# Kernel optimization log

Hardware: AMD Instinct MI355X
Metric: run time of the kernel (lower is better)

Reference implementation:

```python
import jax, jax.numpy as jnp
import numpy as np

B, LQ, D, H, NL, NP, DFF = 8, 1800, 256, 8, 4, 4, 1024
DH = D // H
SHAPES = np.array([[100, 150], [50, 75], [25, 38], [13, 19]], dtype=np.int64)
LIN = int((SHAPES[:, 0] * SHAPES[:, 1]).sum())
QN, QP = -8.0, 7.0  # 4-bit signed LSQ


def lsq(w, alpha):
    """LSQ weight quantization (per-tensor scale, STE round/grad-scale)."""
    g = 1.0 / jnp.sqrt(w.size * QP)
    a = alpha * g + jax.lax.stop_gradient(alpha - alpha * g)  # grad-scaled alpha
    wn = jnp.clip(w / a, QN, QP)
    wq = wn + jax.lax.stop_gradient(jnp.round(wn) - wn)       # round with STE
    return wq * a


def linear_q(x, w, b, a):
    return x @ lsq(w, a).T + b


def layer_norm(x, g, b, eps=1e-5):
    m = x.mean(-1, keepdims=True)
    v = ((x - m) ** 2).mean(-1, keepdims=True)
    return (x - m) / jnp.sqrt(v + eps) * g + b


def setup_inputs():
    key = jax.random.key(0)
    ks = list(jax.random.split(key, 20))

    def nrm(i, shape, s=0.02):
        return jax.random.normal(ks[i], shape, jnp.float32) * s

    def alpha(w):
        return 2.0 * jnp.mean(jnp.abs(w)) / jnp.sqrt(QP)

    qW, kW, vW, oW = nrm(0, (D, D)), nrm(1, (D, D)), nrm(2, (D, D)), nrm(3, (D, D))
    val_W = nrm(4, (D, D))
    off_W = nrm(5, (H * NL * NP * 2, D))
    aw_W = nrm(6, (H * NL * NP, D))
    out_W = nrm(7, (D, D))
    W1, W2 = nrm(8, (DFF, D)), nrm(9, (D, DFF))
    lsi = np.concatenate([[0], np.cumsum(SHAPES[:, 0] * SHAPES[:, 1])[:-1]]).astype(np.int64)
    z = jnp.zeros
    return dict(
        tgt=nrm(10, (B, LQ, D), 1.0),
        query_pos=nrm(11, (B, LQ, D), 1.0),
        reference_points=jax.random.uniform(ks[12], (B, LQ, NL, 2), jnp.float32),
        src=nrm(13, (B, LIN, D), 1.0),
        qW=qW, qb=z(D), kW=kW, kb=z(D), vW=vW, vb=z(D), oW=oW, ob=z(D),
        a_q=alpha(qW), a_k=alpha(kW), a_v=alpha(vW), a_o=alpha(oW),
        val_W=val_W, val_b=z(D), a_val=alpha(val_W),
        off_W=off_W, off_b=z(H * NL * NP * 2),
        aw_W=aw_W, aw_b=z(H * NL * NP),
        out_W=out_W, out_b=z(D), a_out=alpha(out_W),
        W1=W1, b1=z(DFF), a_w1=alpha(W1),
        W2=W2, b2=z(D), a_w2=alpha(W2),
        ln1_g=jnp.ones(D), ln1_b=z(D),
        ln2_g=jnp.ones(D), ln2_b=z(D),
        ln3_g=jnp.ones(D), ln3_b=z(D),
        src_spatial_shapes=jnp.asarray(SHAPES),
        level_start_index=jnp.asarray(lsi),
        src_padding_mask=jnp.zeros((B, LIN), dtype=bool),
    )


def reference(tgt, query_pos, reference_points, src,
              qW, qb, kW, kb, vW, vb, oW, ob, a_q, a_k, a_v, a_o,
              val_W, val_b, a_val, off_W, off_b, aw_W, aw_b, out_W, out_b, a_out,
              W1, b1, a_w1, W2, b2, a_w2,
              ln1_g, ln1_b, ln2_g, ln2_b, ln3_g, ln3_b,
              src_spatial_shapes, level_start_index, src_padding_mask):
    shapes = np.asarray(src_spatial_shapes)  # static spatial shapes per level

    # ---- quantized self-attention (dropout = eval mode, i.e. identity) ----
    qk_in = tgt + query_pos
    q = linear_q(qk_in, qW, qb, a_q).reshape(B, LQ, H, DH)
    k = linear_q(qk_in, kW, kb, a_k).reshape(B, LQ, H, DH)
    v = linear_q(tgt, vW, vb, a_v).reshape(B, LQ, H, DH)
    scores = jnp.einsum('bqhd,bkhd->bhqk', q, k) / jnp.sqrt(jnp.float32(DH))
    p = jax.nn.softmax(scores, axis=-1)
    sa = jnp.einsum('bhqk,bkhd->bqhd', p, v).reshape(B, LQ, D)
    tgt = layer_norm(tgt + linear_q(sa, oW, ob, a_o), ln2_g, ln2_b)

    # ---- quantized multi-scale deformable cross-attention ----
    query = tgt + query_pos
    value = linear_q(src, val_W, val_b, a_val)
    value = jnp.where(src_padding_mask[..., None], 0.0, value)
    value = value.reshape(B, LIN, H, DH)
    offs = (query @ off_W.T + off_b).reshape(B, LQ, H, NL, NP, 2)
    aw = (query @ aw_W.T + aw_b).reshape(B, LQ, H, NL * NP)
    aw = jax.nn.softmax(aw, axis=-1).reshape(B, LQ, H, NL, NP)
    # offset normalizer is (W_l, H_l)
    norm = jnp.asarray(shapes[:, ::-1].astype(np.float32))  # [NL, 2]
    loc = reference_points[:, :, None, :, None, :] + offs / norm[None, None, None, :, None, :]

    bidx = jnp.arange(B)[:, None, None, None]
    hidx = jnp.arange(H)[None, None, :, None]
    acc = jnp.zeros((B, LQ, H, DH), jnp.float32)
    start = 0
    for l in range(NL):
        Hl, Wl = int(shapes[l, 0]), int(shapes[l, 1])
        v_l = jax.lax.dynamic_slice_in_dim(value, start, Hl * Wl, 1).reshape(B, Hl, Wl, H, DH)
        # grid_sample semantics: align_corners=False, zero padding
        x = loc[:, :, :, l, :, 0] * Wl - 0.5  # [B, LQ, H, NP]
        y = loc[:, :, :, l, :, 1] * Hl - 0.5
        x0 = jnp.floor(x); y0 = jnp.floor(y)
        x0i = x0.astype(jnp.int32); y0i = y0.astype(jnp.int32)
        wx1 = x - x0; wy1 = y - y0
        wx0 = 1.0 - wx1; wy0 = 1.0 - wy1

        def gather(yi, xi):
            valid = (yi >= 0) & (yi < Hl) & (xi >= 0) & (xi < Wl)
            yc = jnp.clip(yi, 0, Hl - 1); xc = jnp.clip(xi, 0, Wl - 1)
            g = v_l[bidx, yc, xc, hidx]  # [B, LQ, H, NP, DH]
            return g * valid[..., None]

        samp = (gather(y0i, x0i) * (wy0 * wx0)[..., None]
                + gather(y0i, x0i + 1) * (wy0 * wx1)[..., None]
                + gather(y0i + 1, x0i) * (wy1 * wx0)[..., None]
                + gather(y0i + 1, x0i + 1) * (wy1 * wx1)[..., None])
        acc = acc + (aw[:, :, :, l, :, None] * samp).sum(axis=3)
        start += Hl * Wl

    ca = linear_q(acc.reshape(B, LQ, D), out_W, out_b, a_out)
    tgt = layer_norm(tgt + ca, ln1_g, ln1_b)

    # ---- quantized FFN ----
    t2 = linear_q(jax.nn.relu(linear_q(tgt, W1, b1, a_w1)), W2, b2, a_w2)
    tgt = layer_norm(tgt + t2, ln3_g, ln3_b)
    return tgt
```

## Files before the change

### kernel.cpp

```cpp
#include <hip/hip_runtime.h>
#include <hip/hip_bf16.h>

static constexpr int B_   = 8;
static constexpr int LQ_  = 1800;
static constexpr int D_   = 256;
static constexpr int H_   = 8;
static constexpr int DFF_ = 1024;
static constexpr int LIN_ = 19947;
static constexpr int MQ_  = B_ * LQ_;
static constexpr int NELEM_ = MQ_ * D_;

#define CDIV(a, b) (((a) + (b) - 1) / (b))

typedef unsigned short u16;
typedef unsigned int   u32;
typedef unsigned long long u64;
typedef __attribute__((ext_vector_type(8))) __bf16 bf16x8;
typedef __attribute__((ext_vector_type(4))) float  f32x4;
typedef __attribute__((ext_vector_type(4))) u32    u32x4;

#if __has_builtin(__builtin_amdgcn_exp2f)
#define EXP2(x) __builtin_amdgcn_exp2f(x)
#else
#define EXP2(x) exp2f(x)
#endif

__device__ __forceinline__ u16 f2bf(float f) {
    union { __bf16 h; u16 u; } v; v.h = (__bf16)f; return v.u;
}
__device__ __forceinline__ float bf2f(u16 u) {
    union { u32 u; float f; } v; v.u = ((u32)u) << 16;
    return v.f;
}

__device__ __forceinline__ f32x4 mfma_bf16(bf16x8 a, bf16x8 b, f32x4 c) {
    return __builtin_amdgcn_mfma_f32_16x16x32_bf16(a, b, c, 0, 0, 0);
}

__device__ __forceinline__ void gload16(const void* g, void* l) {
    __builtin_amdgcn_global_load_lds(
        (const __attribute__((address_space(1))) void*)g,
        (__attribute__((address_space(3))) void*)l,
        16, 0, 0);
}

template <int N> __device__ __forceinline__ void waitvm() {
    if constexpr (N == 0) asm volatile("s_waitcnt vmcnt(0)" ::: "memory");
    else if constexpr (N == 3) asm volatile("s_waitcnt vmcnt(3)" ::: "memory");
    else if constexpr (N == 4) asm volatile("s_waitcnt vmcnt(4)" ::: "memory");
    else if constexpr (N == 5) asm volatile("s_waitcnt vmcnt(5)" ::: "memory");
    else if constexpr (N == 6) asm volatile("s_waitcnt vmcnt(6)" ::: "memory");
}

__global__ void k_quant(const float* __restrict__ w, const float* __restrict__ alpha,
                        u16* __restrict__ o, int n) {
    int i = blockIdx.x * blockDim.x + threadIdx.x;
    if (i >= n) return;
    float a = alpha[0];
    float wn = fminf(fmaxf(w[i] / a, -8.f), 7.f);
    o[i] = f2bf(rintf(wn) * a);
}

__global__ void k_cvt(const float* __restrict__ w, u16* __restrict__ o, int n) {
    int i = blockIdx.x * blockDim.x + threadIdx.x;
    if (i < n) o[i] = f2bf(w[i]);
}

__global__ void k_addcvt(const float* __restrict__ a, const float* __restrict__ b,
                         u16* __restrict__ o, int n) {
    int i = blockIdx.x * blockDim.x + threadIdx.x;
    if (i < n) o[i] = f2bf(a[i] + b[i]);
}

__global__ void k_addcvt2(const u16* __restrict__ a, const float* __restrict__ b,
                          u16* __restrict__ o, int n) {
    int i = blockIdx.x * blockDim.x + threadIdx.x;
    if (i < n) o[i] = f2bf(bf2f(a[i]) + b[i]);
}

struct rawf8 { float4 a, b; };
__device__ __forceinline__ bf16x8 loadraw(const u16* p) { return *(const bf16x8*)p; }
__device__ __forceinline__ rawf8  loadraw(const float* p) {
    rawf8 r; r.a = *(const float4*)p; r.b = *(const float4*)(p + 4); return r;
}
__device__ __forceinline__ void wlds(u16* d, bf16x8 v) { *(bf16x8*)d = v; }
__device__ __forceinline__ void wlds(u16* d, rawf8 v) {
    bf16x8 r;
    r[0] = (__bf16)v.a.x; r[1] = (__bf16)v.a.y; r[2] = (__bf16)v.a.z; r[3] = (__bf16)v.a.w;
    r[4] = (__bf16)v.b.x; r[5] = (__bf16)v.b.y; r[6] = (__bf16)v.b.z; r[7] = (__bf16)v.b.w;
    *(bf16x8*)d = r;
}
__device__ __forceinline__ void storey(float* p, float v) { *p = v; }
__device__ __forceinline__ void storey(u16* p, float v)   { *p = f2bf(v); }

template <typename XT, typename OT, bool RELU, int BN>
__global__ __launch_bounds__(256) void k_gemm3(
    const XT* __restrict__ X, const u16* __restrict__ W,
    const float* __restrict__ bias, OT* __restrict__ Y,
    int M, int N, int K)
{
    constexpr int WN  = BN / 2;
    constexpr int NFR = WN / 16;
    constexpr bool XF32 = (sizeof(XT) == 4);
    constexpr int L = (XF32 ? 2 : 1) + BN / 64;
    constexpr int ASZ = 64 * 32 * (XF32 ? 2 : 1);
    constexpr int BSZ = BN * 32;
    __shared__ __align__(16) u16 As[2][ASZ];
    __shared__ __align__(16) u16 Bs[2][BSZ];

    const int tid = threadIdx.x;
    const int wave = tid >> 6, lane = tid & 63;
    const int wr = wave >> 1, wc = wave & 1;
    const int fr = lane & 15, fg = lane >> 4;
    const int bm = blockIdx.x * 64, bn = blockIdx.y * BN;

    f32x4 acc[2][NFR];
    #pragma unroll
    for (int m = 0; m < 2; ++m)
        #pragma unroll
        for (int n = 0; n < NFR; ++n) acc[m][n] = (f32x4){0.f, 0.f, 0.f, 0.f};

    auto stageA = [&](int buf, int kt) {
        if constexpr (!XF32) {
            int r = (wave << 4) + (lane >> 2);
            int grow = bm + r; if (grow > M - 1) grow = M - 1;
            int cs = (lane & 3) ^ ((lane >> 3) & 3);
            gload16((const u16*)X + (size_t)grow * K + (kt << 5) + (cs << 3),
                    &As[buf][wave * 512]);
        } else {
            float* Af = (float*)As[buf];
            #pragma unroll
            for (int t = 0; t < 2; ++t) {
                int r = (t << 5) + (wave << 3) + (lane >> 3);
                int grow = bm + r; if (grow > M - 1) grow = M - 1;
                int cs = (lane & 7) ^ ((lane >> 3) & 7);
                gload16((const float*)X + (size_t)grow * K + (kt << 5) + (cs << 2),
                        &Af[((t << 5) + (wave << 3)) * 32]);
            }
        }
    };
    auto stageB = [&](int buf, int kt) {
        #pragma unroll
        for (int t = 0; t < BN / 64; ++t) {
            int r = (t << 6) + (wave << 4) + (lane >> 2);
            int cs = (lane & 3) ^ ((lane >> 3) & 3);
            gload16(W + (size_t)(bn + r) * K + (kt << 5) + (cs << 3),
                    &Bs[buf][((t << 6) + (wave << 4)) * 32]);
        }
    };

    stageA(0, 0); stageB(0, 0);

    const int nk = K >> 5;
    int cur = 0;
    for (int kt = 0; kt < nk; ++kt) {
        if (kt + 1 < nk) {
            stageA(cur ^ 1, kt + 1); stageB(cur ^ 1, kt + 1);
            waitvm<L>();
        } else {
            waitvm<0>();
        }
        __builtin_amdgcn_s_barrier();

        bf16x8 af[2], bg[NFR];
        #pragma unroll
        for (int m = 0; m < 2; ++m) {
            int r = wr * 32 + m * 16 + fr;
            if constexpr (!XF32) {
                af[m] = *(const bf16x8*)&As[cur][r * 32 + ((fg ^ ((fr >> 1) & 3)) << 3)];
            } else {
                const float* Af = (const float*)As[cur];
                int s0 = (fg << 1) ^ (fr & 7);
                f32x4 x0 = *(const f32x4*)&Af[r * 32 + (s0 << 2)];
                f32x4 x1 = *(const f32x4*)&Af[r * 32 + ((s0 ^ 1) << 2)];
                #pragma unroll
                for (int j = 0; j < 4; ++j) {
                    af[m][j]     = (__bf16)x0[j];
                    af[m][4 + j] = (__bf16)x1[j];
                }
            }
        }
        #pragma unroll
        for (int n = 0; n < NFR; ++n) {
            int r = wc * WN + n * 16 + fr;
            bg[n] = *(const bf16x8*)&Bs[cur][r * 32 + ((fg ^ ((fr >> 1) & 3)) << 3)];
        }
        #pragma unroll
        for (int m = 0; m < 2; ++m)
            #pragma unroll
            for (int n = 0; n < NFR; ++n)
                acc[m][n] = mfma_bf16(af[m], bg[n], acc[m][n]);

        __builtin_amdgcn_s_barrier();
        cur ^= 1;
    }

    #pragma unroll
    for (int m = 0; m < 2; ++m) {
        #pragma unroll
        for (int i = 0; i < 4; ++i) {
            int grow = bm + wr * 32 + m * 16 + fg * 4 + i;
            if (grow >= M) continue;
            #pragma unroll
            for (int n = 0; n < NFR; ++n) {
                int gcol = bn + wc * WN + n * 16 + fr;
                float v = acc[m][n][i] + bias[gcol];
                if (RELU) v = fmaxf(v, 0.f);
                storey(Y + (size_t)grow * N + gcol, v);
            }
        }
    }
}

template <typename XT, typename OT, bool RELU>
__global__ __launch_bounds__(256) void k_gemm(
    const XT* __restrict__ X, const u16* __restrict__ W,
    const float* __restrict__ bias, OT* __restrict__ Y,
    int M, int N, int K)
{
    __shared__ u16 Ash[128 * 40];
    __shared__ u16 Bsh[128 * 40];
    const int tid = threadIdx.x;
    const int wave = tid >> 6, lane = tid & 63;
    const int wr = wave >> 1, wc = wave & 1;
    const int fr = lane & 15, fg = lane >> 4;
    const int bm = blockIdx.x * 128, bn = blockIdx.y * 128;
    const int srow = tid >> 2, sc = (tid & 3) * 8;

    f32x4 acc[4][4];
    #pragma unroll
    for (int m = 0; m < 4; ++m)
        #pragma unroll
        for (int n = 0; n < 4; ++n) acc[m][n] = (f32x4){0.f, 0.f, 0.f, 0.f};

    for (int k0 = 0; k0 < K; k0 += 32) {
        __syncthreads();
        #pragma unroll
        for (int i = 0; i < 2; ++i) {
            int row = srow + i * 64;
            int gr = bm + row; if (gr > M - 1) gr = M - 1;
            wlds(&Ash[row * 40 + sc], loadraw(X + (size_t)gr * K + k0 + sc));
            int wn = bn + row; if (wn > N - 1) wn = N - 1;
            wlds(&Bsh[row * 40 + sc], loadraw(W + (size_t)wn * K + k0 + sc));
        }
        __syncthreads();
        bf16x8 af[4], bg[4];
        #pragma unroll
        for (int m = 0; m < 4; ++m)
            af[m] = *(const bf16x8*)&Ash[(wr * 64 + m * 16 + fr) * 40 + fg * 8];
        #pragma unroll
        for (int n = 0; n < 4; ++n)
            bg[n] = *(const bf16x8*)&Bsh[(wc * 64 + n * 16 + fr) * 40 + fg * 8];
        #pragma unroll
        for (int m = 0; m < 4; ++m)
            #pragma unroll
            for (int n = 0; n < 4; ++n)
                acc[m][n] = mfma_bf16(af[m], bg[n], acc[m][n]);
    }

    #pragma unroll
    for (int m = 0; m < 4; ++m) {
        #pragma unroll
        for (int i = 0; i < 4; ++i) {
            int grow = bm + wr * 64 + m * 16 + fg * 4 + i;
            if (grow >= M) continue;
            #pragma unroll
            for (int n = 0; n < 4; ++n) {
                int gcol = bn + wc * 64 + n * 16 + fr;
                if (gcol >= N) continue;
                float v = acc[m][n][i] + bias[gcol];
                if (RELU) v = fmaxf(v, 0.f);
                storey(Y + (size_t)grow * N + gcol, v);
            }
        }
    }
}

__global__ __launch_bounds__(256) void k_attn(
    const u16* __restrict__ Q, const u16* __restrict__ K,
    const u16* __restrict__ V, u16* __restrict__ O)
{
    __shared__ u16 Ks[128 * 40];
    __shared__ u16 Vt[32 * 136];
    const int b = blockIdx.z, h = blockIdx.y;
    const int q0 = blockIdx.x * 64;
    const int tid = threadIdx.x;
    const int wave = tid >> 6, lane = tid & 63;
    const int fr = lane & 15, fg = lane >> 4;
    constexpr float C2 = 0.25503486f;

    int qg = q0 + wave * 16 + fr; if (qg >= LQ_) qg = LQ_ - 1;
    bf16x8 qf;
    {
        bf16x8 qraw = *(const bf16x8*)&Q[((size_t)(b * LQ_ + qg)) * 256 + h * 32 + fg * 8];
        #pragma unroll
        for (int j = 0; j < 8; ++j) qf[j] = (__bf16)((float)qraw[j] * C2);
    }

    const bf16x8 ones = {(__bf16)1.f, (__bf16)1.f, (__bf16)1.f, (__bf16)1.f,
                         (__bf16)1.f, (__bf16)1.f, (__bf16)1.f, (__bf16)1.f};

    f32x4 o0 = (f32x4){0.f,0.f,0.f,0.f}, o1 = (f32x4){0.f,0.f,0.f,0.f};
    f32x4 lacc = (f32x4){0.f,0.f,0.f,0.f};

    const int kr = tid >> 1, kc = (tid & 1) * 16;
    const int vp = lane, vdh = wave * 8;
    const int cp = ((vp >> 4) << 4) | (((vp >> 1) & 3) << 2) | (((vp >> 3) & 1) << 1) | (vp & 1);

    for (int kb0 = 0; kb0 < LQ_; kb0 += 128) {
        const bool tail = (kb0 + 128 > LQ_);
        __syncthreads();
        {
            int kg = kb0 + kr; if (kg >= LQ_) kg = LQ_ - 1;
            const u16* kp = &K[((size_t)(b * LQ_ + kg)) * 256 + h * 32 + kc];
            *(bf16x8*)&Ks[kr * 40 + kc]     = *(const bf16x8*)kp;
            *(bf16x8*)&Ks[kr * 40 + kc + 8] = *(const bf16x8*)(kp + 8);
            int v0 = kb0 + 2 * vp, v1 = v0 + 1;
            if (v0 >= LQ_) v0 = LQ_ - 1;
            if (v1 >= LQ_) v1 = LQ_ - 1;
            union { bf16x8 v; u16 s[8]; } va, vb2;
            va.v  = *(const bf16x8*)&V[((size_t)(b * LQ_ + v0)) * 256 + h * 32 + vdh];
            vb2.v = *(const bf16x8*)&V[((size_t)(b * LQ_ + v1)) * 256 + h * 32 + vdh];
            #pragma unroll
            for (int j = 0; j < 8; ++j)
                *(u32*)&Vt[(vdh + j) * 136 + 2 * cp] = (u32)va.s[j] | ((u32)vb2.s[j] << 16);
        }
        __syncthreads();

        u32x4 pq[4];
        #pragma unroll
        for (int f = 0; f < 8; ++f) {
            bf16x8 ka = *(const bf16x8*)&Ks[(f * 16 + fr) * 40 + fg * 8];
            f32x4 s = mfma_bf16(ka, qf, (f32x4){0.f,0.f,0.f,0.f});
            if (tail) {
                #pragma unroll
                for (int i = 0; i < 4; ++i)
                    if (kb0 + f * 16 + fg * 4 + i >= LQ_) s[i] = -3e38f;
            }
            float p0 = EXP2(s[0]), p1 = EXP2(s[1]);
            float p2 = EXP2(s[2]), p3 = EXP2(s[3]);
            union { __bf16 h[2]; u32 w; } c0, c1;
            c0.h[0] = (__bf16)p0; c0.h[1] = (__bf16)p1;
            c1.h[0] = (__bf16)p2; c1.h[1] = (__bf16)p3;
            pq[f >> 1][(f & 1) * 2 + 0] = c0.w;
            pq[f >> 1][(f & 1) * 2 + 1] = c1.w;
        }

        #pragma unroll
        for (int ks = 0; ks < 4; ++ks) {
            bf16x8 pb  = __builtin_bit_cast(bf16x8, pq[ks]);
            bf16x8 va0 = *(const bf16x8*)&Vt[fr * 136 + ks * 32 + fg * 8];
            bf16x8 va1 = *(const bf16x8*)&Vt[(16 + fr) * 136 + ks * 32 + fg * 8];
            o0 = mfma_bf16(va0, pb, o0);
            o1 = mfma_bf16(va1, pb, o1);
            lacc = mfma_bf16(ones, pb, lacc);
        }
    }

    float inv = 1.f / lacc[0];
    int qout = q0 + wave * 16 + fr;
    if (qout < LQ_) {
        size_t base = ((size_t)(b * LQ_ + qout)) * 256 + h * 32;
        #pragma unroll
        for (int i = 0; i < 4; ++i) {
            O[base + fg * 4 + i]      = f2bf(o0[i] * inv);
            O[base + 16 + fg * 4 + i] = f2bf(o1[i] * inv);
        }
    }
}

__device__ __forceinline__ float ldf(const float* p) { return *p; }
__device__ __forceinline__ float ldf(const u16* p)   { return bf2f(*p); }

template <typename RT, typename OT>
__global__ __launch_bounds__(256) void k_resln(
    const u16* __restrict__ X, const RT* __restrict__ R,
    const float* __restrict__ g, const float* __restrict__ bb,
    OT* __restrict__ O)
{
    const int row = blockIdx.x;
    const int d = threadIdx.x;
    const size_t off = (size_t)row * D_ + d;
    float v = ldf(R + off) + bf2f(X[off]);
    __shared__ float r1[4], r2[4];
    int lane = d & 63, wid = d >> 6;
    float s = v;
    #pragma unroll
    for (int o_ = 32; o_ >= 1; o_ >>= 1) s += __shfl_xor(s, o_);
    if (lane == 0) r1[wid] = s;
    __syncthreads();
    float mean = (r1[0] + r1[1] + r1[2] + r1[3]) * (1.f / 256.f);
    float dv = v - mean;
    float sq = dv * dv;
    #pragma unroll
    for (int o_ = 32; o_ >= 1; o_ >>= 1) sq += __shfl_xor(sq, o_);
    if (lane == 0) r2[wid] = sq;
    __syncthreads();
    float var = (r2[0] + r2[1] + r2[2] + r2[3]) * (1.f / 256.f);
    storey(O + off, dv / sqrtf(var + 1e-5f) * g[d] + bb[d]);
}

__global__ __launch_bounds__(256) void k_sample(
    const float* __restrict__ offs, const float* __restrict__ aw,
    const u16* __restrict__ value, const float* __restrict__ refp,
    u16* __restrict__ acc_out)
{
    __shared__ u32 pts[2][128][8];
    const int t = threadIdx.x;
    const int bq0 = blockIdx.x * 2;
    const int b = bq0 / LQ_;

    constexpr int Hl[4] = {100, 50, 25, 13};
    constexpr int Wl[4] = {150, 75, 38, 19};
    constexpr int LS[4] = {0, 15000, 18750, 19700};

    {
        const int qsub = t >> 7;
        const int pt = t & 127;
        const int h = pt >> 4, lp = pt & 15;
        const int l = lp >> 2, p = lp & 3;
        const int bq = bq0 + qsub;

        float2 oxy = *(const float2*)&offs[(size_t)bq * 256 + h * 32 + l * 8 + p * 2];
        float av = aw[(size_t)bq * 128 + h * 16 + lp];
        float mx = av;
        #pragma unroll
        for (int s = 1; s < 16; s <<= 1) mx = fmaxf(mx, __shfl_xor(mx, s));
        float e = __expf(av - mx);
        float sum = e;
        #pragma unroll
        for (int s = 1; s < 16; s <<= 1) sum += __shfl_xor(sum, s);
        float a = e / sum;

        float2 rxy = *(const float2*)&refp[(size_t)bq * 8 + l * 2];
        const float Wf = (float)Wl[l], Hf = (float)Hl[l];
        float x = (rxy.x + oxy.x / Wf) * Wf - 0.5f;
        float y = (rxy.y + oxy.y / Hf) * Hf - 0.5f;
        float x0f = floorf(x), y0f = floorf(y);
        int x0 = (int)x0f, y0 = (int)y0f;
        float wx1 = x - x0f, wy1 = y - y0f;
        float wx0 = 1.f - wx1, wy0 = 1.f - wy1;

        u32 ov[4]; float wv[4];
        #pragma unroll
        for (int c = 0; c < 4; ++c) {
            int cy = c >> 1, cx = c & 1;
            int yi = y0 + cy, xi = x0 + cx;
            bool valid = (yi >= 0) && (yi < Hl[l]) && (xi >= 0) && (xi < Wl[l]);
            ov[c] = valid ? (u32)((LS[l] + yi * Wl[l] + xi) * 256 + h * 32) : 0u;
            float w = (cy ? wy1 : wy0) * (cx ? wx1 : wx0) * a;
            wv[c] = valid ? w : 0.f;
        }
        u32* dst = pts[qsub][lp * 8 + h];
        *(uint4*)dst = make_uint4(ov[0], ov[1], ov[2], ov[3]);
        float4 wq = make_float4(wv[0], wv[1], wv[2], wv[3]);
        *(float4*)(dst + 4) = wq;
    }
    __syncthreads();

    const int qsub = t >> 7;
    const int h = (t >> 4) & 7;
    const int dp = t & 15;
    const u16* vb = value + (size_t)b * LIN_ * 256 + 2 * dp;
    float a0 = 0.f, a1 = 0.f;
    #pragma unroll
    for (int i = 0; i < 16; ++i) {
        const u32* P = pts[qsub][i * 8 + h];
        uint4 o4 = *(const uint4*)P;
        float4 w4 = *(const float4*)(P + 4);
        u32 g;
        g = *(const u32*)&vb[o4.x]; a0 += w4.x * bf2f((u16)g); a1 += w4.x * bf2f((u16)(g >> 16));
        g = *(const u32*)&vb[o4.y]; a0 += w4.y * bf2f((u16)g); a1 += w4.y * bf2f((u16)(g >> 16));
        g = *(const u32*)&vb[o4.z]; a0 += w4.z * bf2f((u16)g); a1 += w4.z * bf2f((u16)(g >> 16));
        g = *(const u32*)&vb[o4.w]; a0 += w4.w * bf2f((u16)g); a1 += w4.w * bf2f((u16)(g >> 16));
    }
    const int bq = bq0 + qsub;
    u32 packed = (u32)f2bf(a0) | ((u32)f2bf(a1) << 16);
    *(u32*)&acc_out[(size_t)bq * 256 + h * 32 + 2 * dp] = packed;
}

extern "C" void kernel_launch(void* const* d_in, const int* in_sizes, int n_in,
                              void* d_out, int out_size, void* d_ws, size_t ws_size,
                              hipStream_t stream)
{
    (void)in_sizes; (void)n_in; (void)out_size; (void)ws_size;
    const float* tgt   = (const float*)d_in[0];
    const float* qpos  = (const float*)d_in[1];
    const float* refp  = (const float*)d_in[2];
    const float* src   = (const float*)d_in[3];
    const float* qW    = (const float*)d_in[4];
    const float* qb    = (const float*)d_in[5];
    const float* kW    = (const float*)d_in[6];
    const float* kb    = (const float*)d_in[7];
    const float* vW    = (const float*)d_in[8];
    const float* vb    = (const float*)d_in[9];
    const float* oW    = (const float*)d_in[10];
    const float* ob    = (const float*)d_in[11];
    const float* a_q   = (const float*)d_in[12];
    const float* a_k   = (const float*)d_in[13];
    const float* a_v   = (const float*)d_in[14];
    const float* a_o   = (const float*)d_in[15];
    const float* val_W = (const float*)d_in[16];
    const float* val_b = (const float*)d_in[17];
    const float* a_val = (const float*)d_in[18];
    const float* off_W = (const float*)d_in[19];
    const float* off_b = (const float*)d_in[20];
    const float* aw_W  = (const float*)d_in[21];
    const float* aw_b  = (const float*)d_in[22];
    const float* out_W = (const float*)d_in[23];
    const float* out_b = (const float*)d_in[24];
    const float* a_out = (const float*)d_in[25];
    const float* W1    = (const float*)d_in[26];
    const float* b1    = (const float*)d_in[27];
    const float* a_w1  = (const float*)d_in[28];
    const float* W2    = (const float*)d_in[29];
    const float* b2    = (const float*)d_in[30];
    const float* a_w2  = (const float*)d_in[31];
    const float* ln1_g = (const float*)d_in[32];
    const float* ln1_b = (const float*)d_in[33];
    const float* ln2_g = (const float*)d_in[34];
    const float* ln2_b = (const float*)d_in[35];
    const float* ln3_g = (const float*)d_in[36];
    const float* ln3_b = (const float*)d_in[37];

    u16* wq_q  = (u16*)d_ws;
    u16* wq_k  = wq_q + 65536;
    u16* wq_v  = wq_k + 65536;
    u16* wq_o  = wq_v + 65536;
    u16* wq_vl = wq_o + 65536;
    u16* wq_ot = wq_vl + 65536;
    u16* w_off = wq_ot + 65536;
    u16* w_aw  = w_off + 65536;
    u16* wq_1  = w_aw + 32768;
    u16* wq_2  = wq_1 + 262144;
    u16* bufA  = wq_2 + 262144;
    u16* bufB  = bufA + NELEM_;
    u16* bufC  = bufB + NELEM_;
    u16* bufD  = bufC + NELEM_;
    u16* bufE  = bufD + NELEM_;
    float* offs = (float*)(bufE + NELEM_);
    float* awb  = offs + NELEM_;
    u16* valb   = (u16*)(awb + MQ_ * 128);

    const int TB = 256;
    const int MVAL = B_ * LIN_;
    const int GM = MQ_ / 64;
    const int GV = CDIV(MVAL, 64);

    k_quant<<<CDIV(65536, TB), TB, 0, stream>>>(qW, a_q, wq_q, 65536);
    k_quant<<<CDIV(65536, TB), TB, 0, stream>>>(kW, a_k, wq_k, 65536);
    k_quant<<<CDIV(65536, TB), TB, 0, stream>>>(vW, a_v, wq_v, 65536);
    k_quant<<<CDIV(65536, TB), TB, 0, stream>>>(oW, a_o, wq_o, 65536);
    k_quant<<<CDIV(65536, TB), TB, 0, stream>>>(val_W, a_val, wq_vl, 65536);
    k_quant<<<CDIV(65536, TB), TB, 0, stream>>>(out_W, a_out, wq_ot, 65536);
    k_quant<<<CDIV(262144, TB), TB, 0, stream>>>(W1, a_w1, wq_1, 262144);
    k_quant<<<CDIV(262144, TB), TB, 0, stream>>>(W2, a_w2, wq_2, 262144);
    k_cvt<<<CDIV(65536, TB), TB, 0, stream>>>(off_W, w_off, 65536);
    k_cvt<<<CDIV(32768, TB), TB, 0, stream>>>(aw_W, w_aw, 32768);

    k_addcvt<<<CDIV(NELEM_, TB), TB, 0, stream>>>(tgt, qpos, bufA, NELEM_);
    k_cvt<<<CDIV(NELEM_, TB), TB, 0, stream>>>(tgt, bufB, NELEM_);

    k_gemm3<u16, u16, false, 128><<<dim3(GM, 2), TB, 0, stream>>>(bufA, wq_q, qb, bufC, MQ_, 256, 256);
    k_gemm3<u16, u16, false, 128><<<dim3(GM, 2), TB, 0, stream>>>(bufA, wq_k, kb, bufD, MQ_, 256, 256);
    k_gemm3<u16, u16, false, 128><<<dim3(GM, 2), TB, 0, stream>>>(bufB, wq_v, vb, bufE, MQ_, 256, 256);
    k_attn<<<dim3(CDIV(LQ_,64), H_, B_), TB, 0, stream>>>(bufC, bufD, bufE, bufA);
    k_gemm3<u16, u16, false, 128><<<dim3(GM, 2), TB, 0, stream>>>(bufA, wq_o, ob, bufB, MQ_, 256, 256);
    k_resln<float, u16><<<MQ_, TB, 0, stream>>>(bufB, tgt, ln2_g, ln2_b, bufC);

    k_addcvt2<<<CDIV(NELEM_, TB), TB, 0, stream>>>(bufC, qpos, bufD, NELEM_);
    k_gemm3<float, u16, false, 128><<<dim3(GV, 2), TB, 0, stream>>>(src, wq_vl, val_b, valb, MVAL, 256, 256);
    k_gemm3<u16, float, false, 128><<<dim3(GM, 2), TB, 0, stream>>>(bufD, w_off, off_b, offs, MQ_, 256, 256);
    k_gemm<u16, float, false><<<dim3(CDIV(MQ_,128), 1), TB, 0, stream>>>(bufD, w_aw, aw_b, awb, MQ_, 128, 256);
    k_sample<<<MQ_ / 2, TB, 0, stream>>>(offs, awb, valb, refp, bufE);
    k_gemm3<u16, u16, false, 128><<<dim3(GM, 2), TB, 0, stream>>>(bufE, wq_ot, out_b, bufA, MQ_, 256, 256);
    k_resln<u16, u16><<<MQ_, TB, 0, stream>>>(bufA, bufC, ln1_g, ln1_b, bufB);

    u16* ffn1 = valb;
    k_gemm3<u16, u16, true , 128><<<dim3(GM, 8), TB, 0, stream>>>(bufB, wq_1, b1, ffn1, MQ_, 1024, 256);
    k_gemm3<u16, u16, false, 128><<<dim3(GM, 2), TB, 0, stream>>>(ffn1, wq_2, b2, bufD, MQ_, 256, 1024);
    k_resln<u16, float><<<MQ_, TB, 0, stream>>>(bufD, bufB, ln3_g, ln3_b, (float*)d_out);
}
```

Before: 401.9 us.

## Fuse weight prep kernels, merge Q/K and offset/attn-weight GEMMs

Replaces the ten per-weight quantize/convert launches with a single prep kernel that also packs the fused biases. The Q and K projections become one N=512 GEMM, and the offset and attention-weight projections become one N=384 GEMM, so k_attn and k_sample read from interleaved buffers. The two tgt conversion kernels are merged into one, and the value projection uses a BN=256 tile. The aim is fewer launches and less repeated reading of the activation matrix, at the cost of wider, strided output rows and a long branch chain in the prep kernel.

Result: faster. 340.3 us (-15.3%).

```diff
diff --git a/kernel.cpp b/kernel.cpp
--- a/kernel.cpp
+++ b/kernel.cpp
@@ -52,24 +52,44 @@
     else if constexpr (N == 6) asm volatile("s_waitcnt vmcnt(6)" ::: "memory");
 }
 
-__global__ void k_quant(const float* __restrict__ w, const float* __restrict__ alpha,
-                        u16* __restrict__ o, int n) {
+__global__ void k_prep(
+    const float* __restrict__ qW,   const float* __restrict__ kW,
+    const float* __restrict__ vW,   const float* __restrict__ oW,
+    const float* __restrict__ valW, const float* __restrict__ outW,
+    const float* __restrict__ W1,   const float* __restrict__ W2,
+    const float* __restrict__ offW, const float* __restrict__ awW,
+    const float* __restrict__ a_q,  const float* __restrict__ a_k,
+    const float* __restrict__ a_v,  const float* __restrict__ a_o,
+    const float* __restrict__ a_val,const float* __restrict__ a_out,
+    const float* __restrict__ a_w1, const float* __restrict__ a_w2,
+    const float* __restrict__ qb,   const float* __restrict__ kb,
+    const float* __restrict__ off_b,const float* __restrict__ aw_b,
+    u16* __restrict__ wout, float* __restrict__ bout)
+{
+    int i = blockIdx.x * 256 + threadIdx.x;
+    auto q8 = [&](const float* w, const float* al, int off) {
+        float a = al[0];
+        float wn = fminf(fmaxf(w[off] / a, -8.f), 7.f);
+        wout[i] = f2bf(rintf(wn) * a);
+    };
+    if      (i <   65536) q8(qW,   a_q,   i);
+    else if (i <  131072) q8(kW,   a_k,   i -   65536);
+    else if (i <  196608) q8(vW,   a_v,   i -  131072);
+    else if (i <  262144) q8(oW,   a_o,   i -  196608);
+    else if (i <  327680) q8(valW, a_val, i -  262144);
+    else if (i <  393216) q8(outW, a_out, i -  327680);
+    else if (i <  655360) q8(W1,   a_w1,  i -  393216);
+    else if (i <  917504) q8(W2,   a_w2,  i -  655360);
+    else if (i <  983040) wout[i] = f2bf(offW[i - 917504]);
+    else if (i < 1015808) wout[i] = f2bf(awW[i - 983040]);
+    else if (i < 1016320) { int j = i - 1015808; bout[j]       = (j < 256) ? qb[j]    : kb[j - 256];  }
+    else if (i < 1016704) { int j = i - 1016320; bout[512 + j] = (j < 256) ? off_b[j] : aw_b[j - 256]; }
+}
+
+__global__ void k_tgtprep(const float* __restrict__ tgt, const float* __restrict__ qpos,
+                          u16* __restrict__ A, u16* __restrict__ Bb, int n) {
     int i = blockIdx.x * blockDim.x + threadIdx.x;
-    if (i >= n) return;
-    float a = alpha[0];
-    float wn = fminf(fmaxf(w[i] / a, -8.f), 7.f);
-    o[i] = f2bf(rintf(wn) * a);
-}
-
-__global__ void k_cvt(const float* __restrict__ w, u16* __restrict__ o, int n) {
-    int i = blockIdx.x * blockDim.x + threadIdx.x;
-    if (i < n) o[i] = f2bf(w[i]);
-}
-
-__global__ void k_addcvt(const float* __restrict__ a, const float* __restrict__ b,
-                         u16* __restrict__ o, int n) {
-    int i = blockIdx.x * blockDim.x + threadIdx.x;
-    if (i < n) o[i] = f2bf(a[i] + b[i]);
+    if (i < n) { float t = tgt[i]; A[i] = f2bf(t + qpos[i]); Bb[i] = f2bf(t); }
 }
 
 __global__ void k_addcvt2(const u16* __restrict__ a, const float* __restrict__ b,
@@ -78,18 +98,6 @@
     if (i < n) o[i] = f2bf(bf2f(a[i]) + b[i]);
 }
 
-struct rawf8 { float4 a, b; };
-__device__ __forceinline__ bf16x8 loadraw(const u16* p) { return *(const bf16x8*)p; }
-__device__ __forceinline__ rawf8  loadraw(const float* p) {
-    rawf8 r; r.a = *(const float4*)p; r.b = *(const float4*)(p + 4); return r;
-}
-__device__ __forceinline__ void wlds(u16* d, bf16x8 v) { *(bf16x8*)d = v; }
-__device__ __forceinline__ void wlds(u16* d, rawf8 v) {
-    bf16x8 r;
-    r[0] = (__bf16)v.a.x; r[1] = (__bf16)v.a.y; r[2] = (__bf16)v.a.z; r[3] = (__bf16)v.a.w;
-    r[4] = (__bf16)v.b.x; r[5] = (__bf16)v.b.y; r[6] = (__bf16)v.b.z; r[7] = (__bf16)v.b.w;
-    *(bf16x8*)d = r;
-}
 __device__ __forceinline__ void storey(float* p, float v) { *p = v; }
 __device__ __forceinline__ void storey(u16* p, float v)   { *p = f2bf(v); }
 
@@ -212,73 +220,8 @@
     }
 }
 
-template <typename XT, typename OT, bool RELU>
-__global__ __launch_bounds__(256) void k_gemm(
-    const XT* __restrict__ X, const u16* __restrict__ W,
-    const float* __restrict__ bias, OT* __restrict__ Y,
-    int M, int N, int K)
-{
-    __shared__ u16 Ash[128 * 40];
-    __shared__ u16 Bsh[128 * 40];
-    const int tid = threadIdx.x;
-    const int wave = tid >> 6, lane = tid & 63;
-    const int wr = wave >> 1, wc = wave & 1;
-    const int fr = lane & 15, fg = lane >> 4;
-    const int bm = blockIdx.x * 128, bn = blockIdx.y * 128;
-    const int srow = tid >> 2, sc = (tid & 3) * 8;
-
-    f32x4 acc[4][4];
-    #pragma unroll
-    for (int m = 0; m < 4; ++m)
-        #pragma unroll
-        for (int n = 0; n < 4; ++n) acc[m][n] = (f32x4){0.f, 0.f, 0.f, 0.f};
-
-    for (int k0 = 0; k0 < K; k0 += 32) {
-        __syncthreads();
-        #pragma unroll
-        for (int i = 0; i < 2; ++i) {
-            int row = srow + i * 64;
-            int gr = bm + row; if (gr > M - 1) gr = M - 1;
-            wlds(&Ash[row * 40 + sc], loadraw(X + (size_t)gr * K + k0 + sc));
-            int wn = bn + row; if (wn > N - 1) wn = N - 1;
-            wlds(&Bsh[row * 40 + sc], loadraw(W + (size_t)wn * K + k0 + sc));
-        }
-        __syncthreads();
-        bf16x8 af[4], bg[4];
-        #pragma unroll
-        for (int m = 0; m < 4; ++m)
-            af[m] = *(const bf16x8*)&Ash[(wr * 64 + m * 16 + fr) * 40 + fg * 8];
-        #pragma unroll
-        for (int n = 0; n < 4; ++n)
-            bg[n] = *(const bf16x8*)&Bsh[(wc * 64 + n * 16 + fr) * 40 + fg * 8];
-        #pragma unroll
-        for (int m = 0; m < 4; ++m)
-            #pragma unroll
-            for (int n = 0; n < 4; ++n)
-                acc[m][n] = mfma_bf16(af[m], bg[n], acc[m][n]);
-    }
-
-    #pragma unroll
-    for (int m = 0; m < 4; ++m) {
-        #pragma unroll
-        for (int i = 0; i < 4; ++i) {
-            int grow = bm + wr * 64 + m * 16 + fg * 4 + i;
-            if (grow >= M) continue;
-            #pragma unroll
-            for (int n = 0; n < 4; ++n) {
-                int gcol = bn + wc * 64 + n * 16 + fr;
-                if (gcol >= N) continue;
-                float v = acc[m][n][i] + bias[gcol];
-                if (RELU) v = fmaxf(v, 0.f);
-                storey(Y + (size_t)grow * N + gcol, v);
-            }
-        }
-    }
-}
-
 __global__ __launch_bounds__(256) void k_attn(
-    const u16* __restrict__ Q, const u16* __restrict__ K,
-    const u16* __restrict__ V, u16* __restrict__ O)
+    const u16* __restrict__ QK, const u16* __restrict__ V, u16* __restrict__ O)
 {
     __shared__ u16 Ks[128 * 40];
     __shared__ u16 Vt[32 * 136];
@@ -292,7 +235,7 @@
     int qg = q0 + wave * 16 + fr; if (qg >= LQ_) qg = LQ_ - 1;
     bf16x8 qf;
     {
-        bf16x8 qraw = *(const bf16x8*)&Q[((size_t)(b * LQ_ + qg)) * 256 + h * 32 + fg * 8];
+        bf16x8 qraw = *(const bf16x8*)&QK[((size_t)(b * LQ_ + qg)) * 512 + h * 32 + fg * 8];
         #pragma unroll
         for (int j = 0; j < 8; ++j) qf[j] = (__bf16)((float)qraw[j] * C2);
     }
@@ -312,7 +255,7 @@
         __syncthreads();
         {
             int kg = kb0 + kr; if (kg >= LQ_) kg = LQ_ - 1;
-            const u16* kp = &K[((size_t)(b * LQ_ + kg)) * 256 + h * 32 + kc];
+            const u16* kp = &QK[((size_t)(b * LQ_ + kg)) * 512 + 256 + h * 32 + kc];
             *(bf16x8*)&Ks[kr * 40 + kc]     = *(const bf16x8*)kp;
             *(bf16x8*)&Ks[kr * 40 + kc + 8] = *(const bf16x8*)(kp + 8);
             int v0 = kb0 + 2 * vp, v1 = v0 + 1;
@@ -401,7 +344,7 @@
 }
 
 __global__ __launch_bounds__(256) void k_sample(
-    const float* __restrict__ offs, const float* __restrict__ aw,
+    const float* __restrict__ oaw,
     const u16* __restrict__ value, const float* __restrict__ refp,
     u16* __restrict__ acc_out)
 {
@@ -421,8 +364,8 @@
         const int l = lp >> 2, p = lp & 3;
         const int bq = bq0 + qsub;
 
-        float2 oxy = *(const float2*)&offs[(size_t)bq * 256 + h * 32 + l * 8 + p * 2];
-        float av = aw[(size_t)bq * 128 + h * 16 + lp];
+        float2 oxy = *(const float2*)&oaw[(size_t)bq * 384 + h * 32 + l * 8 + p * 2];
+        float av = oaw[(size_t)bq * 384 + 256 + h * 16 + lp];
         float mx = av;
         #pragma unroll
         for (int s = 1; s < 16; s <<= 1) mx = fmaxf(mx, __shfl_xor(mx, s));
@@ -523,56 +466,45 @@
     const float* ln3_g = (const float*)d_in[36];
     const float* ln3_b = (const float*)d_in[37];
 
-    u16* wq_q  = (u16*)d_ws;
-    u16* wq_k  = wq_q + 65536;
-    u16* wq_v  = wq_k + 65536;
-    u16* wq_o  = wq_v + 65536;
-    u16* wq_vl = wq_o + 65536;
-    u16* wq_ot = wq_vl + 65536;
-    u16* w_off = wq_ot + 65536;
-    u16* w_aw  = w_off + 65536;
-    u16* wq_1  = w_aw + 32768;
-    u16* wq_2  = wq_1 + 262144;
-    u16* bufA  = wq_2 + 262144;
-    u16* bufB  = bufA + NELEM_;
-    u16* bufC  = bufB + NELEM_;
-    u16* bufD  = bufC + NELEM_;
-    u16* bufE  = bufD + NELEM_;
-    float* offs = (float*)(bufE + NELEM_);
-    float* awb  = offs + NELEM_;
-    u16* valb   = (u16*)(awb + MQ_ * 128);
+    u16* wbase = (u16*)d_ws;
+    u16* wq_q  = wbase;
+    u16* wq_v  = wbase + 131072;
+    u16* wq_o  = wbase + 196608;
+    u16* wq_vl = wbase + 262144;
+    u16* wq_ot = wbase + 327680;
+    u16* wq_1  = wbase + 393216;
+    u16* wq_2  = wbase + 655360;
+    u16* w_off = wbase + 917504;
+    float* bfused = (float*)(wbase + 1015808);
+    u16* bufA = (u16*)(bfused + 1024);
+    u16* bufB = bufA + NELEM_;
+    u16* bufC = bufB + NELEM_;
+    u16* bufD = bufC + NELEM_;
+    u16* bufE = bufD + NELEM_;
+    float* oaw = (float*)(bufE + NELEM_);
+    u16* valb  = (u16*)(oaw + (size_t)MQ_ * 384);
 
     const int TB = 256;
     const int MVAL = B_ * LIN_;
     const int GM = MQ_ / 64;
     const int GV = CDIV(MVAL, 64);
 
-    k_quant<<<CDIV(65536, TB), TB, 0, stream>>>(qW, a_q, wq_q, 65536);
-    k_quant<<<CDIV(65536, TB), TB, 0, stream>>>(kW, a_k, wq_k, 65536);
-    k_quant<<<CDIV(65536, TB), TB, 0, stream>>>(vW, a_v, wq_v, 65536);
-    k_quant<<<CDIV(65536, TB), TB, 0, stream>>>(oW, a_o, wq_o, 65536);
-    k_quant<<<CDIV(65536, TB), TB, 0, stream>>>(val_W, a_val, wq_vl, 65536);
-    k_quant<<<CDIV(65536, TB), TB, 0, stream>>>(out_W, a_out, wq_ot, 65536);
-    k_quant<<<CDIV(262144, TB), TB, 0, stream>>>(W1, a_w1, wq_1, 262144);
-    k_quant<<<CDIV(262144, TB), TB, 0, stream>>>(W2, a_w2, wq_2, 262144);
-    k_cvt<<<CDIV(65536, TB), TB, 0, stream>>>(off_W, w_off, 65536);
-    k_cvt<<<CDIV(32768, TB), TB, 0, stream>>>(aw_W, w_aw, 32768);
-
-    k_addcvt<<<CDIV(NELEM_, TB), TB, 0, stream>>>(tgt, qpos, bufA, NELEM_);
-    k_cvt<<<CDIV(NELEM_, TB), TB, 0, stream>>>(tgt, bufB, NELEM_);
-
-    k_gemm3<u16, u16, false, 128><<<dim3(GM, 2), TB, 0, stream>>>(bufA, wq_q, qb, bufC, MQ_, 256, 256);
-    k_gemm3<u16, u16, false, 128><<<dim3(GM, 2), TB, 0, stream>>>(bufA, wq_k, kb, bufD, MQ_, 256, 256);
+    k_prep<<<CDIV(1016704, TB), TB, 0, stream>>>(
+        qW, kW, vW, oW, val_W, out_W, W1, W2, off_W, aw_W,
+        a_q, a_k, a_v, a_o, a_val, a_out, a_w1, a_w2,
+        qb, kb, off_b, aw_b, wbase, bfused);
+    k_tgtprep<<<CDIV(NELEM_, TB), TB, 0, stream>>>(tgt, qpos, bufA, bufB, NELEM_);
+
+    k_gemm3<u16, u16, false, 128><<<dim3(GM, 4), TB, 0, stream>>>(bufA, wq_q, bfused, bufC, MQ_, 512, 256);
     k_gemm3<u16, u16, false, 128><<<dim3(GM, 2), TB, 0, stream>>>(bufB, wq_v, vb, bufE, MQ_, 256, 256);
-    k_attn<<<dim3(CDIV(LQ_,64), H_, B_), TB, 0, stream>>>(bufC, bufD, bufE, bufA);
-    k_gemm3<u16, u16, false, 128><<<dim3(GM, 2), TB, 0, stream>>>(bufA, wq_o, ob, bufB, MQ_, 256, 256);
-    k_resln<float, u16><<<MQ_, TB, 0, stream>>>(bufB, tgt, ln2_g, ln2_b, bufC);
+    k_attn<<<dim3(CDIV(LQ_,64), H_, B_), TB, 0, stream>>>(bufC, bufE, bufA);
+    k_gemm3<u16, u16, false, 128><<<dim3(GM, 2), TB, 0, stream>>>(bufA, wq_o, ob, bufD, MQ_, 256, 256);
+    k_resln<float, u16><<<MQ_, TB, 0, stream>>>(bufD, tgt, ln2_g, ln2_b, bufC);
 
     k_addcvt2<<<CDIV(NELEM_, TB), TB, 0, stream>>>(bufC, qpos, bufD, NELEM_);
-    k_gemm3<float, u16, false, 128><<<dim3(GV, 2), TB, 0, stream>>>(src, wq_vl, val_b, valb, MVAL, 256, 256);
-    k_gemm3<u16, float, false, 128><<<dim3(GM, 2), TB, 0, stream>>>(bufD, w_off, off_b, offs, MQ_, 256, 256);
-    k_gemm<u16, float, false><<<dim3(CDIV(MQ_,128), 1), TB, 0, stream>>>(bufD, w_aw, aw_b, awb, MQ_, 128, 256);
-    k_sample<<<MQ_ / 2, TB, 0, stream>>>(offs, awb, valb, refp, bufE);
+    k_gemm3<float, u16, false, 256><<<dim3(GV, 1), TB, 0, stream>>>(src, wq_vl, val_b, valb, MVAL, 256, 256);
+    k_gemm3<u16, float, false, 128><<<dim3(GM, 3), TB, 0, stream>>>(bufD, w_off, bfused + 512, oaw, MQ_, 384, 256);
+    k_sample<<<MQ_ / 2, TB, 0, stream>>>(oaw, valb, refp, bufE);
     k_gemm3<u16, u16, false, 128><<<dim3(GM, 2), TB, 0, stream>>>(bufE, wq_ot, out_b, bufA, MQ_, 256, 256);
     k_resln<u16, u16><<<MQ_, TB, 0, stream>>>(bufA, bufC, ln1_g, ln1_b, bufB);
 
```
